# Kernel optimization log

Hardware: AMD Instinct MI355X
Metric: run time of the kernel (lower is better)

The kernel has to match this reference:

```python
import jax, jax.numpy as jnp
import numpy as np

B = 2097152  # batch rows
NBITS = 64
NCTRL = 6


def setup_inputs() -> dict:
    key = jax.random.key(0)
    k1, k2 = jax.random.split(key)
    # binary pulse inputs (0/1), matching the spiking-logic representation
    data = jnp.round(jax.random.uniform(k1, (B, NBITS), dtype=jnp.float32))
    shift = jnp.round(jax.random.uniform(k2, (B, NCTRL), dtype=jnp.float32))
    return {"data": data, "shift": shift}


def reference(data, shift):
    """64-wide barrel shifter: 6 mux stages, shift bit 5-i controls stage with
    shift_amount 1<<i (MSB-first control word). Output bit k = input bit k - s
    when selected, zero-filled at the low end — exactly the torch loop's math,
    vectorized over all 64 lanes per stage."""
    current = data
    for i in range(6):
        s = shift[..., 5 - i:6 - i]          # [B, 1] select bit for this stage
        sa = 1 << i                           # shift amount of this stage
        zeros = jnp.zeros_like(current[..., :sa])
        shifted = jnp.concatenate([zeros, current[..., :-sa]], axis=-1)  # [B, 64]
        # MUXGate(sel, a, b) = sel*a + (1-sel)*b, applied to all 64 lanes at once
        current = s * shifted + (1.0 - s) * current
    return current
```

## Files before the change

kernel.cpp:

```cpp
#include <hip/hip_runtime.h>


typedef float f4 __attribute__((ext_vector_type(4)));

__device__ __forceinline__ f4 rowshift(f4 val, unsigned long long b,
                                       int g, int t16) {
    unsigned sub = (unsigned)(b >> (6 * g)) & 63u;
    int S = (int)(__brev(sub) >> 26);
    int q0 = t16 * 4 - S;
    int t = q0 & 3;

    bool b0 = (t & 1) != 0, b1 = (t & 2) != 0;
    float r0 = b1 ? val.z : val.x;
    float r1 = b1 ? val.w : val.y;
    float r2 = b1 ? val.x : val.z;
    float r3 = b1 ? val.y : val.w;
    float s0 = b0 ? r1 : r0;
    float s1 = b0 ? r2 : r1;
    float s2 = b0 ? r3 : r2;
    float s3 = b0 ? r0 : r3;

    int la0 = (q0    ) >> 2;
    int la1 = (q0 + 1) >> 2;
    int la2 = (q0 + 2) >> 2;
    int la3 = (q0 + 3) >> 2;
    la0 = la0 < 0 ? 0 : la0;
    la1 = la1 < 0 ? 0 : la1;
    la2 = la2 < 0 ? 0 : la2;
    la3 = la3 < 0 ? 0 : la3;
    int base = g * 16;

    float o0 = __shfl(s0, base + la0, 64);
    float o1 = __shfl(s1, base + la1, 64);
    float o2 = __shfl(s2, base + la2, 64);
    float o3 = __shfl(s3, base + la3, 64);

    o0 = (q0 >= 0)  ? o0 : 0.0f;
    o1 = (q0 >= -1) ? o1 : 0.0f;
    o2 = (q0 >= -2) ? o2 : 0.0f;
    o3 = (q0 >= -3) ? o3 : 0.0f;
    f4 r;
    r.x = o0; r.y = o1; r.z = o2; r.w = o3;
    return r;
}

__global__ __launch_bounds__(256)
void BarrelShifterRight64_kernel(const float* __restrict__ data,
                                 const float* __restrict__ shift,
                                 float* __restrict__ out,
                                 int nwrows) {
    const int lane = threadIdx.x & 63;
    const int wib  = threadIdx.x >> 6;
    const int wpb  = blockDim.x >> 6;
    const int nw   = gridDim.x * wpb;
    const int w0   = blockIdx.x * wpb + wib;

    const f4* __restrict__ d4 = (const f4*)data;
    f4* __restrict__       o4 = (f4*)out;

    const int g   = lane >> 4;
    const int t16 = lane & 15;

    for (int w = w0; w < nwrows; w += 2 * nw) {
        const int w1 = w + nw;
        const bool have1 = w1 < nwrows;

        f4 vA = __builtin_nontemporal_load(&d4[w * 64 + lane]);
        float svA = (lane < 24) ? shift[w * 24 + lane] : 0.0f;

        f4 vB = (f4)(0.0f);
        float svB = 0.0f;
        if (have1) {
            vB  = __builtin_nontemporal_load(&d4[w1 * 64 + lane]);
            svB = (lane < 24) ? shift[w1 * 24 + lane] : 0.0f;
        }

        unsigned long long bA = __ballot(svA > 0.5f);
        f4 oA = rowshift(vA, bA, g, t16);
        __builtin_nontemporal_store(oA, &o4[w * 64 + lane]);

        if (have1) {
            unsigned long long bB = __ballot(svB > 0.5f);
            f4 oB = rowshift(vB, bB, g, t16);
            __builtin_nontemporal_store(oB, &o4[w1 * 64 + lane]);
        }
    }
}

extern "C" void kernel_launch(void* const* d_in, const int* in_sizes, int n_in,
                              void* d_out, int out_size, void* d_ws, size_t ws_size,
                              hipStream_t stream) {
    const float* data  = (const float*)d_in[0];
    const float* shift = (const float*)d_in[1];
    float* out = (float*)d_out;

    const int nrows  = in_sizes[0] / 64;
    const int nwrows = nrows / 4;

    const int block = 256;
    const int grid  = 2048;
    BarrelShifterRight64_kernel<<<grid, block, 0, stream>>>(data, shift, out, nwrows);
}
```

Measured before the change: 203.2 us.

## Replace shuffle-based row shift with direct unaligned shifted global loads, prefetch shift bits

Instead of loading each row aligned and realigning it with lane shuffles and selects, each lane now computes its shift amount first and loads its four output floats directly from the input at the shifted (possibly unaligned) offset. Out-of-range elements at the low end are zeroed. The shift-control values for the next iteration are also prefetched a loop iteration ahead. This removes the cross-lane shuffles but makes data loads depend on the shift load, produces unaligned and misaligned memory accesses, and drops the nontemporal hint on input loads.

After: 204.5 us. About the same (+0.6%).

```diff
diff --git a/kernel.cpp b/kernel.cpp
--- a/kernel.cpp
+++ b/kernel.cpp
@@ -3,45 +3,26 @@
 
 typedef float f4 __attribute__((ext_vector_type(4)));
 
-__device__ __forceinline__ f4 rowshift(f4 val, unsigned long long b,
-                                       int g, int t16) {
-    unsigned sub = (unsigned)(b >> (6 * g)) & 63u;
-    int S = (int)(__brev(sub) >> 26);
-    int q0 = t16 * 4 - S;
-    int t = q0 & 3;
-
-    bool b0 = (t & 1) != 0, b1 = (t & 2) != 0;
-    float r0 = b1 ? val.z : val.x;
-    float r1 = b1 ? val.w : val.y;
-    float r2 = b1 ? val.x : val.z;
-    float r3 = b1 ? val.y : val.w;
-    float s0 = b0 ? r1 : r0;
-    float s1 = b0 ? r2 : r1;
-    float s2 = b0 ? r3 : r2;
-    float s3 = b0 ? r0 : r3;
-
-    int la0 = (q0    ) >> 2;
-    int la1 = (q0 + 1) >> 2;
-    int la2 = (q0 + 2) >> 2;
-    int la3 = (q0 + 3) >> 2;
-    la0 = la0 < 0 ? 0 : la0;
-    la1 = la1 < 0 ? 0 : la1;
-    la2 = la2 < 0 ? 0 : la2;
-    la3 = la3 < 0 ? 0 : la3;
-    int base = g * 16;
-
-    float o0 = __shfl(s0, base + la0, 64);
-    float o1 = __shfl(s1, base + la1, 64);
-    float o2 = __shfl(s2, base + la2, 64);
-    float o3 = __shfl(s3, base + la3, 64);
-
-    o0 = (q0 >= 0)  ? o0 : 0.0f;
-    o1 = (q0 >= -1) ? o1 : 0.0f;
-    o2 = (q0 >= -2) ? o2 : 0.0f;
-    o3 = (q0 >= -3) ? o3 : 0.0f;
-    f4 r;
-    r.x = o0; r.y = o1; r.z = o2; r.w = o3;
-    return r;
+__device__ __forceinline__ f4 shifted_load(const float* __restrict__ data,
+                                           int rowbase, int q0) {
+    int fidx  = rowbase + q0;
+    int fidxc = fidx < 0 ? 0 : fidx;
+    f4 v;
+    __builtin_memcpy(&v, data + fidxc, 16);
+    f4 o;
+    o.x = (q0 >= 0)  ? v.x : 0.0f;
+    o.y = (q0 >= -1) ? v.y : 0.0f;
+    o.z = (q0 >= -2) ? v.z : 0.0f;
+    o.w = (q0 >= -3) ? v.w : 0.0f;
+    if (fidx < 0) {
+        int p1 = q0 + 1, p2 = q0 + 2, p3 = q0 + 3;
+        float e0 = v.x, e1 = v.y, e2 = v.z;
+        o.x = 0.0f;
+        o.y = (p1 == 0) ? e0 : ((p1 == 1) ? e1 : ((p1 == 2) ? e2 : 0.0f));
+        o.z = (p2 == 0) ? e0 : ((p2 == 1) ? e1 : ((p2 == 2) ? e2 : 0.0f));
+        o.w = (p3 == 0) ? e0 : ((p3 == 1) ? e1 : ((p3 == 2) ? e2 : 0.0f));
+    }
+    return o;
 }
 
 __global__ __launch_bounds__(256)
@@ -55,35 +36,42 @@
     const int nw   = gridDim.x * wpb;
     const int w0   = blockIdx.x * wpb + wib;
 
-    const f4* __restrict__ d4 = (const f4*)data;
-    f4* __restrict__       o4 = (f4*)out;
+    f4* __restrict__ o4 = (f4*)out;
 
     const int g   = lane >> 4;
     const int t16 = lane & 15;
+    const bool sl = lane < 24;
+
+    int wA = w0, wB = w0 + nw;
+    float svA = (sl && wA < nwrows) ? shift[wA * 24 + lane] : 0.0f;
+    float svB = (sl && wB < nwrows) ? shift[wB * 24 + lane] : 0.0f;
 
     for (int w = w0; w < nwrows; w += 2 * nw) {
         const int w1 = w + nw;
         const bool have1 = w1 < nwrows;
 
-        f4 vA = __builtin_nontemporal_load(&d4[w * 64 + lane]);
-        float svA = (lane < 24) ? shift[w * 24 + lane] : 0.0f;
+        unsigned long long bA = __ballot(svA > 0.5f);
+        unsigned long long bB = __ballot(svB > 0.5f);
 
-        f4 vB = (f4)(0.0f);
-        float svB = 0.0f;
+        const int wA2 = w + 2 * nw, wB2 = w + 3 * nw;
+        svA = (sl && wA2 < nwrows) ? shift[wA2 * 24 + lane] : 0.0f;
+        svB = (sl && wB2 < nwrows) ? shift[wB2 * 24 + lane] : 0.0f;
+
+        unsigned subA = (unsigned)(bA >> (6 * g)) & 63u;
+        int SA  = (int)(__brev(subA) >> 26);
+        int q0A = t16 * 4 - SA;
+        f4 oA = shifted_load(data, w * 256 + g * 64, q0A);
+
+        f4 oB;
         if (have1) {
-            vB  = __builtin_nontemporal_load(&d4[w1 * 64 + lane]);
-            svB = (lane < 24) ? shift[w1 * 24 + lane] : 0.0f;
+            unsigned subB = (unsigned)(bB >> (6 * g)) & 63u;
+            int SB  = (int)(__brev(subB) >> 26);
+            int q0B = t16 * 4 - SB;
+            oB = shifted_load(data, w1 * 256 + g * 64, q0B);
         }
 
-        unsigned long long bA = __ballot(svA > 0.5f);
-        f4 oA = rowshift(vA, bA, g, t16);
         __builtin_nontemporal_store(oA, &o4[w * 64 + lane]);
-
-        if (have1) {
-            unsigned long long bB = __ballot(svB > 0.5f);
-            f4 oB = rowshift(vB, bB, g, t16);
-            __builtin_nontemporal_store(oB, &o4[w1 * 64 + lane]);
-        }
+        if (have1) __builtin_nontemporal_store(oB, &o4[w1 * 64 + lane]);
     }
 }
 
```

## Unroll row loop by four with prefetched shift bits and exact-fit fast path

Applied to the files above, without the earlier changes.

Adds a specialised kernel that handles four wave-rows per iteration when the row count divides evenly by the grid stride. It prefetches the next iteration's shift words while the current iteration's data is processed, so more loads are in flight and the bounds checks disappear. Otherwise it falls back to a simple one-row-per-iteration kernel. It costs more registers and code size, and part of the speed-up depends on the exact-divisibility path being taken.

New measurement: 239.3 us. +17.7%, slower.

```diff
diff --git a/kernel.cpp b/kernel.cpp
--- a/kernel.cpp
+++ b/kernel.cpp
@@ -20,14 +20,10 @@
     float s2 = b0 ? r3 : r2;
     float s3 = b0 ? r0 : r3;
 
-    int la0 = (q0    ) >> 2;
-    int la1 = (q0 + 1) >> 2;
-    int la2 = (q0 + 2) >> 2;
-    int la3 = (q0 + 3) >> 2;
-    la0 = la0 < 0 ? 0 : la0;
-    la1 = la1 < 0 ? 0 : la1;
-    la2 = la2 < 0 ? 0 : la2;
-    la3 = la3 < 0 ? 0 : la3;
+    int la0 = (q0    ) >> 2;  la0 = la0 < 0 ? 0 : la0;
+    int la1 = (q0 + 1) >> 2;  la1 = la1 < 0 ? 0 : la1;
+    int la2 = (q0 + 2) >> 2;  la2 = la2 < 0 ? 0 : la2;
+    int la3 = (q0 + 3) >> 2;  la3 = la3 < 0 ? 0 : la3;
     int base = g * 16;
 
     float o0 = __shfl(s0, base + la0, 64);
@@ -35,20 +31,20 @@
     float o2 = __shfl(s2, base + la2, 64);
     float o3 = __shfl(s3, base + la3, 64);
 
-    o0 = (q0 >= 0)  ? o0 : 0.0f;
-    o1 = (q0 >= -1) ? o1 : 0.0f;
-    o2 = (q0 >= -2) ? o2 : 0.0f;
-    o3 = (q0 >= -3) ? o3 : 0.0f;
     f4 r;
-    r.x = o0; r.y = o1; r.z = o2; r.w = o3;
+    r.x = (q0 >= 0)  ? o0 : 0.0f;
+    r.y = (q0 >= -1) ? o1 : 0.0f;
+    r.z = (q0 >= -2) ? o2 : 0.0f;
+    r.w = (q0 >= -3) ? o3 : 0.0f;
     return r;
 }
 
 __global__ __launch_bounds__(256)
-void BarrelShifterRight64_kernel(const float* __restrict__ data,
-                                 const float* __restrict__ shift,
-                                 float* __restrict__ out,
-                                 int nwrows) {
+void BarrelShifterRight64_exact(const float* __restrict__ data,
+                                const float* __restrict__ shift,
+                                float* __restrict__ out,
+                                int nwrows) {
+    constexpr int U = 4;
     const int lane = threadIdx.x & 63;
     const int wib  = threadIdx.x >> 6;
     const int wpb  = blockDim.x >> 6;
@@ -60,30 +56,70 @@
 
     const int g   = lane >> 4;
     const int t16 = lane & 15;
+    const bool sl = lane < 24;
 
-    for (int w = w0; w < nwrows; w += 2 * nw) {
-        const int w1 = w + nw;
-        const bool have1 = w1 < nwrows;
+    const int stride = U * nw;
+    const int niter  = nwrows / stride;
 
-        f4 vA = __builtin_nontemporal_load(&d4[w * 64 + lane]);
-        float svA = (lane < 24) ? shift[w * 24 + lane] : 0.0f;
+    float sv0 = sl ? shift[(w0 + 0 * nw) * 24 + lane] : 0.0f;
+    float sv1 = sl ? shift[(w0 + 1 * nw) * 24 + lane] : 0.0f;
+    float sv2 = sl ? shift[(w0 + 2 * nw) * 24 + lane] : 0.0f;
+    float sv3 = sl ? shift[(w0 + 3 * nw) * 24 + lane] : 0.0f;
 
-        f4 vB = (f4)(0.0f);
-        float svB = 0.0f;
-        if (have1) {
-            vB  = __builtin_nontemporal_load(&d4[w1 * 64 + lane]);
-            svB = (lane < 24) ? shift[w1 * 24 + lane] : 0.0f;
-        }
+    int w = w0;
+    for (int it = 0; it < niter; ++it, w += stride) {
+        unsigned long long b0 = __ballot(sv0 > 0.5f);
+        unsigned long long b1 = __ballot(sv1 > 0.5f);
+        unsigned long long b2 = __ballot(sv2 > 0.5f);
+        unsigned long long b3 = __ballot(sv3 > 0.5f);
 
-        unsigned long long bA = __ballot(svA > 0.5f);
-        f4 oA = rowshift(vA, bA, g, t16);
-        __builtin_nontemporal_store(oA, &o4[w * 64 + lane]);
+        f4 v0 = __builtin_nontemporal_load(&d4[(w + 0 * nw) * 64 + lane]);
+        f4 v1 = __builtin_nontemporal_load(&d4[(w + 1 * nw) * 64 + lane]);
+        f4 v2 = __builtin_nontemporal_load(&d4[(w + 2 * nw) * 64 + lane]);
+        f4 v3 = __builtin_nontemporal_load(&d4[(w + 3 * nw) * 64 + lane]);
 
-        if (have1) {
-            unsigned long long bB = __ballot(svB > 0.5f);
-            f4 oB = rowshift(vB, bB, g, t16);
-            __builtin_nontemporal_store(oB, &o4[w1 * 64 + lane]);
-        }
+        const bool more = it + 1 < niter;
+        const int  wn   = w + stride;
+        sv0 = (sl && more) ? shift[(wn + 0 * nw) * 24 + lane] : 0.0f;
+        sv1 = (sl && more) ? shift[(wn + 1 * nw) * 24 + lane] : 0.0f;
+        sv2 = (sl && more) ? shift[(wn + 2 * nw) * 24 + lane] : 0.0f;
+        sv3 = (sl && more) ? shift[(wn + 3 * nw) * 24 + lane] : 0.0f;
+
+        f4 q0 = rowshift(v0, b0, g, t16);
+        __builtin_nontemporal_store(q0, &o4[(w + 0 * nw) * 64 + lane]);
+        f4 q1 = rowshift(v1, b1, g, t16);
+        __builtin_nontemporal_store(q1, &o4[(w + 1 * nw) * 64 + lane]);
+        f4 q2 = rowshift(v2, b2, g, t16);
+        __builtin_nontemporal_store(q2, &o4[(w + 2 * nw) * 64 + lane]);
+        f4 q3 = rowshift(v3, b3, g, t16);
+        __builtin_nontemporal_store(q3, &o4[(w + 3 * nw) * 64 + lane]);
+    }
+}
+
+__global__ __launch_bounds__(256)
+void BarrelShifterRight64_generic(const float* __restrict__ data,
+                                  const float* __restrict__ shift,
+                                  float* __restrict__ out,
+                                  int nwrows) {
+    const int lane = threadIdx.x & 63;
+    const int wib  = threadIdx.x >> 6;
+    const int wpb  = blockDim.x >> 6;
+    const int nw   = gridDim.x * wpb;
+    const int w0   = blockIdx.x * wpb + wib;
+
+    const f4* __restrict__ d4 = (const f4*)data;
+    f4* __restrict__       o4 = (f4*)out;
+
+    const int g   = lane >> 4;
+    const int t16 = lane & 15;
+    const bool sl = lane < 24;
+
+    for (int w = w0; w < nwrows; w += nw) {
+        float sv = sl ? shift[w * 24 + lane] : 0.0f;
+        unsigned long long b = __ballot(sv > 0.5f);
+        f4 v = __builtin_nontemporal_load(&d4[w * 64 + lane]);
+        f4 o = rowshift(v, b, g, t16);
+        __builtin_nontemporal_store(o, &o4[w * 64 + lane]);
     }
 }
 
@@ -99,5 +135,11 @@
 
     const int block = 256;
     const int grid  = 2048;
-    BarrelShifterRight64_kernel<<<grid, block, 0, stream>>>(data, shift, out, nwrows);
+    const int nw    = grid * (block / 64);
+
+    if (nwrows % (4 * nw) == 0) {
+        BarrelShifterRight64_exact<<<grid, block, 0, stream>>>(data, shift, out, nwrows);
+    } else {
+        BarrelShifterRight64_generic<<<grid, block, 0, stream>>>(data, shift, out, nwrows);
+    }
 }
```
